# Optimization experiments

Hardware: AMD Instinct MI355X
Metric: run time of the kernel (lower is better)

The kernel has to match this reference:

```python
import jax, jax.numpy as jnp
import numpy as np

N = 200000
E = 6400000
NEG_SLOPE = 0.01  # nn.LeakyReLU default

def _leaky(x):
    return jnp.where(x >= 0, x, NEG_SLOPE * x)

def gcn_conv(x, edge_index, W, b, n):
    # PyG GCNConv: add self-loops, symmetric degree norm, linear, scatter-add, bias
    src, dst = edge_index[0], edge_index[1]
    loops = jnp.arange(n, dtype=src.dtype)
    src = jnp.concatenate([src, loops])
    dst = jnp.concatenate([dst, loops])
    deg = jax.ops.segment_sum(jnp.ones_like(dst, dtype=x.dtype), dst, num_segments=n)
    dinv = jnp.where(deg > 0, jax.lax.rsqrt(deg), 0.0)
    norm = dinv[src] * dinv[dst]                  # [E+N]
    h = x @ W.T                                   # [N,50] linear (no bias yet)
    msg = h[src] * norm[:, None]                  # gather + scale
    out = jax.ops.segment_sum(msg, dst, num_segments=n)  # scatter-add to targets
    return out + b

def setup_inputs() -> dict:
    key = jax.random.key(0)
    ks = jax.random.split(key, 20)
    def w(k, o, i):
        return jax.random.normal(k, (o, i), dtype=jnp.float32) * (1.0 / np.sqrt(i))
    def bvec(k, o):
        return jax.random.normal(k, (o,), dtype=jnp.float32) * 0.01
    inp = {
        'x': jax.random.normal(ks[0], (N, 150), dtype=jnp.float32),
        'edge_index': jax.random.randint(ks[1], (2, E), 0, N, dtype=jnp.int64 if jax.config.jax_enable_x64 else jnp.int32),
        'epsilon': jax.random.normal(ks[2], (N, 10), dtype=jnp.float32),
        'Wg': w(ks[3], 50, 50), 'bg': bvec(ks[4], 50),
        'We1': w(ks[5], 40, 50), 'be1': bvec(ks[6], 40),
        'We2': w(ks[7], 30, 40), 'be2': bvec(ks[8], 30),
        'We3': w(ks[9], 20, 30), 'be3': bvec(ks[10], 20),
        'Wfc': w(ks[11], 10, 10), 'bfc': bvec(ks[12], 10),
        'Wd1': w(ks[13], 20, 10), 'bd1': bvec(ks[14], 20),
        'Wd2': w(ks[15], 40, 20), 'bd2': bvec(ks[16], 40),
        'Wd3': w(ks[17], 50, 40), 'bd3': bvec(ks[18], 50),
    }
    return inp

def reference(x, edge_index, epsilon, Wg, bg, We1, be1, We2, be2, We3, be3,
              Wfc, bfc, Wd1, bd1, Wd2, bd2, Wd3, bd3):
    x1 = x[:, 100:]                                   # [N,50]
    h = gcn_conv(x1, edge_index, Wg, bg, x.shape[0])  # [N,50]
    # encoder
    e = _leaky(h @ We1.T + be1)
    e = _leaky(e @ We2.T + be2)
    e = e @ We3.T + be3                               # [N,20]
    mu, log_var = e[:, :10], e[:, 10:]
    # reparameterization: mu + eps * sqrt(exp(log_var))
    z1 = mu + epsilon * jnp.exp(0.5 * log_var)
    z = jax.nn.relu(z1 @ Wfc.T + bfc)                 # FC
    # decoder
    d = _leaky(z @ Wd1.T + bd1)
    d = _leaky(d @ Wd2.T + bd2)
    mu_prime = jax.nn.sigmoid(d @ Wd3.T + bd3)        # [N,50]
    return (mu_prime, mu, log_var, z)
```

## Files before the change

kernel.cpp:

```cpp
#include <hip/hip_runtime.h>


#define NEG 0.01f
#define GS 64
#define ELLS 64
#define SLICES 16
#define SPILL_CAP 65536

#define DET_ES (1024 * 1024)
#define IS64_THRESH (DET_ES / 2)

typedef int vint4 __attribute__((ext_vector_type(4)));

static __device__ __forceinline__ float bf2f(unsigned short u) {
    return __uint_as_float(((unsigned)u) << 16);
}
static __device__ __forceinline__ float leaky(float a) { return (a >= 0.f) ? a : NEG * a; }

__global__ void k_zero(int* __restrict__ indeg, int* __restrict__ flag, int n) {
    int i = blockIdx.x * 256 + threadIdx.x;
    if (i < n) indeg[i] = 0;
    if (i == 0) { flag[0] = 0; flag[1] = 0; flag[2] = 0; }
}

__global__ void k_detect(const unsigned* __restrict__ x, long xwords,
                         const unsigned* __restrict__ ei, long epairs,
                         int* __restrict__ flag) {
    int gw = (blockIdx.x * 256 + threadIdx.x) >> 6;
    int lane = threadIdx.x & 63;
    int side = gw >> 10;
    int ch = gw & 1023;
    int c = 0;
    if (side == 0) {
        long step = xwords >> 10;
        long base = (long)ch * step;
        if (base + 1024 > xwords) base = xwords > 1024 ? xwords - 1024 : 0;
#pragma unroll
        for (int t = 0; t < 16; t++) {
            long idx = base + t * 64 + lane;
            if (idx < xwords) {
                unsigned w = x[idx];
                if (((w >> 23) & 0xFFu) == 0xFFu || ((w >> 7) & 0xFFu) == 0xFFu) c++;
            }
        }
        for (int k = 32; k; k >>= 1) c += __shfl_xor(c, k);
        if (lane == 0 && c) atomicAdd(&flag[0], c);
    } else {
        long step = epairs >> 10;
        long base = (long)ch * step;
        if (base + 1024 > epairs) base = epairs > 1024 ? epairs - 1024 : 0;
#pragma unroll
        for (int t = 0; t < 16; t++) {
            long idx = base + t * 64 + lane;
            if (idx < epairs && ei[2 * idx + 1] == 0u) c++;
        }
        for (int k = 32; k; k >>= 1) c += __shfl_xor(c, k);
        if (lane == 0 && c) atomicAdd(&flag[1], c);
    }
}

__global__ void k_compact(const unsigned* __restrict__ ei, const int* __restrict__ flag,
                          int* __restrict__ src32, int* __restrict__ dst32, long E) {
    bool is64 = flag[1] > IS64_THRESH;
    long i = (long)blockIdx.x * 256 + threadIdx.x;
    const long stride = 2048L * 256;
    if (is64) {
        const int2* p = (const int2*)ei;
        for (; i < E; i += stride) {
            src32[i] = p[i].x;
            dst32[i] = p[E + i].x;
        }
    } else {
        const int* p = (const int*)ei;
        for (; i < E; i += stride) {
            src32[i] = p[i];
            dst32[i] = p[E + i];
        }
    }
}

__global__ __launch_bounds__(256) void k_build(const int* __restrict__ src32,
                        const int* __restrict__ dst32, int* __restrict__ indeg,
                        int* __restrict__ ebuf, int2* __restrict__ spill,
                        int* __restrict__ flag, int E, int N) {
    int blk = blockIdx.x;
    int pass = blk >> 12;
    int xg = blk & 7;
    int q = (blk & 4095) >> 3;
    int s = pass * 8 + xg;
    int sw = (N + SLICES - 1) / SLICES;
    int nlo = s * sw;
    int nhi = nlo + sw; if (nhi > N) nhi = N;
    const long step = 512L * 256 * 4;
    for (long e0 = ((long)q * 256 + threadIdx.x) * 4; e0 < E; e0 += step) {
        int dv[4];
        if (e0 + 4 <= E) {
            vint4 t = __builtin_nontemporal_load((const vint4*)(dst32 + e0));
            dv[0] = t.x; dv[1] = t.y; dv[2] = t.z; dv[3] = t.w;
        } else {
            for (int k = 0; k < 4; k++) dv[k] = (e0 + k < E) ? dst32[e0 + k] : -1;
        }
#pragma unroll
        for (int k = 0; k < 4; k++) {
            int d = dv[k];
            if (d < nlo || d >= nhi) continue;
            int src = __builtin_nontemporal_load(&src32[e0 + k]);
            if ((unsigned)src >= (unsigned)N) continue;
            int c = atomicAdd(&indeg[d], 1);
            if (c < ELLS) {
                ebuf[(size_t)d * ELLS + c] = src;
            } else {
                int o = atomicAdd(&flag[2], 1);
                if (o < SPILL_CAP) spill[o] = make_int2(src, d);
            }
        }
    }
}

__global__ void k_dinv(const int* __restrict__ indeg, float* __restrict__ dinv, int n) {
    int i = blockIdx.x * 256 + threadIdx.x;
    if (i < n) dinv[i] = rsqrtf(1.0f + (float)indeg[i]);
}

struct CW {
    const void* src[16];
    int off[16];
    int n[16];
};
__global__ void k_convw(CW cw, float* __restrict__ dst, const int* __restrict__ flag) {
    int b = blockIdx.x;
    bool isf = flag[0] > 64;
    const float* sf = (const float*)cw.src[b];
    const unsigned short* sh = (const unsigned short*)cw.src[b];
    float* d = dst + cw.off[b];
    int n = cw.n[b];
    for (int i = threadIdx.x; i < n; i += 256) d[i] = isf ? sf[i] : bf2f(sh[i]);
}

#define O_WG 0
#define O_BG 2500
#define O_WE1 2550
#define O_BE1 4550
#define O_WE2 4590
#define O_BE2 5790
#define O_WE3 5820
#define O_BE3 6420
#define O_WFC 6440
#define O_BFC 6540
#define O_WD1 6550
#define O_BD1 6750
#define O_WD2 6770
#define O_BD2 7570
#define O_WD3 7610
#define O_BD3 9610
#define W_TOT 9660

__global__ __launch_bounds__(256) void k_g(const void* __restrict__ xv,
                                           const float* __restrict__ W,
                                           const float* __restrict__ dinv,
                                           const int* __restrict__ flag,
                                           float* __restrict__ g, int n) {
    int i = blockIdx.x * 256 + threadIdx.x;
    if (i >= n) return;
    bool isf = flag[0] > 64;
    float xr[50];
    if (isf) {
        const float* p = (const float*)xv + (size_t)i * 150 + 100;
#pragma unroll
        for (int k = 0; k < 50; k++) xr[k] = p[k];
    } else {
        const unsigned short* p = (const unsigned short*)xv + (size_t)i * 150 + 100;
#pragma unroll
        for (int k = 0; k < 50; k++) xr[k] = bf2f(p[k]);
    }
    const float* Wg = W + O_WG;
    float di = dinv[i];
    float* gr = g + (size_t)i * GS;
#pragma unroll
    for (int f = 0; f < 50; f += 2) {
        float a0 = 0.f, a1 = 0.f;
#pragma unroll
        for (int p = 0; p < 50; p++) {
            a0 += Wg[f * 50 + p] * xr[p];
            a1 += Wg[(f + 1) * 50 + p] * xr[p];
        }
        gr[f] = a0 * di;
        gr[f + 1] = a1 * di;
    }
}

__global__ __launch_bounds__(256) void k_gather(const float* __restrict__ g,
                                                const int* __restrict__ indeg,
                                                const int* __restrict__ ebuf,
                                                const float* __restrict__ dinv,
                                                const float* __restrict__ W,
                                                float* __restrict__ h1, int n) {
    int wid = threadIdx.x >> 6;
    int lane = threadIdx.x & 63;
    int i = blockIdx.x * 4 + wid;
    if (i >= n) return;
    int fc = lane < 50 ? lane : 49;
    int cnt = indeg[i];
    if (cnt > ELLS) cnt = ELLS;
    float di = dinv[i];
    int ev = (lane < cnt) ? ebuf[(size_t)i * ELLS + lane] : 0;
    float a0 = g[(size_t)i * GS + fc];
    float a1 = 0.f, a2 = 0.f, a3 = 0.f, a4 = 0.f, a5 = 0.f, a6 = 0.f, a7 = 0.f;
    int m = 0;
    for (; m + 7 < cnt; m += 8) {
        int j0 = __shfl(ev, m);
        int j1 = __shfl(ev, m + 1);
        int j2 = __shfl(ev, m + 2);
        int j3 = __shfl(ev, m + 3);
        int j4 = __shfl(ev, m + 4);
        int j5 = __shfl(ev, m + 5);
        int j6 = __shfl(ev, m + 6);
        int j7 = __shfl(ev, m + 7);
        a0 += g[(size_t)j0 * GS + fc];
        a1 += g[(size_t)j1 * GS + fc];
        a2 += g[(size_t)j2 * GS + fc];
        a3 += g[(size_t)j3 * GS + fc];
        a4 += g[(size_t)j4 * GS + fc];
        a5 += g[(size_t)j5 * GS + fc];
        a6 += g[(size_t)j6 * GS + fc];
        a7 += g[(size_t)j7 * GS + fc];
    }
    for (; m < cnt; m++) {
        int j = __shfl(ev, m);
        a0 += g[(size_t)j * GS + fc];
    }
    if (lane < 50) {
        float h = (((a0 + a1) + (a2 + a3)) + ((a4 + a5) + (a6 + a7))) * di + W[O_BG + lane];
        h1[(size_t)i * 50 + lane] = h;
    }
}

__global__ void k_spill(const int2* __restrict__ spill, const int* __restrict__ flag,
                        const float* __restrict__ g, const float* __restrict__ dinv,
                        float* __restrict__ h1) {
    int nov = flag[2];
    if (nov > SPILL_CAP) nov = SPILL_CAP;
    int lane = threadIdx.x & 63;
    int wave = (blockIdx.x * 256 + threadIdx.x) >> 6;
    for (int e = wave; e < nov; e += gridDim.x * 4) {
        int2 sd = spill[e];
        if (lane < 50)
            atomicAdd(&h1[(size_t)sd.y * 50 + lane], g[(size_t)sd.x * GS + lane] * dinv[sd.y]);
    }
}


__global__ __launch_bounds__(256) void k_e1(const float* __restrict__ h1,
                                            const float* __restrict__ W,
                                            float* __restrict__ t1, int n) {
    int i = blockIdx.x * 256 + threadIdx.x;
    if (i >= n) return;
    float v0[50];
    const float2* hr = (const float2*)(h1 + (size_t)i * 50);
#pragma unroll
    for (int p = 0; p < 25; p++) {
        float2 q = hr[p];
        v0[2 * p] = q.x;
        v0[2 * p + 1] = q.y;
    }
    float o[40];
#pragma unroll
    for (int f = 0; f < 40; f++) {
        float a = W[O_BE1 + f];
#pragma unroll
        for (int p = 0; p < 50; p++) a += W[O_WE1 + f * 50 + p] * v0[p];
        o[f] = leaky(a);
    }
    float4* ot = (float4*)(t1 + (size_t)i * 40);
#pragma unroll
    for (int p = 0; p < 10; p++) ot[p] = make_float4(o[4 * p], o[4 * p + 1], o[4 * p + 2], o[4 * p + 3]);
}

__global__ __launch_bounds__(256) void k_e23(const float* __restrict__ t1,
                                             const float* __restrict__ W,
                                             float* __restrict__ out, int n) {
    int i = blockIdx.x * 256 + threadIdx.x;
    if (i >= n) return;
    float v1[40];
    const float4* tr = (const float4*)(t1 + (size_t)i * 40);
#pragma unroll
    for (int p = 0; p < 10; p++) {
        float4 q = tr[p];
        v1[4 * p] = q.x; v1[4 * p + 1] = q.y; v1[4 * p + 2] = q.z; v1[4 * p + 3] = q.w;
    }
    float v2[30];
#pragma unroll
    for (int f = 0; f < 30; f++) {
        float a = W[O_BE2 + f];
#pragma unroll
        for (int p = 0; p < 40; p++) a += W[O_WE2 + f * 40 + p] * v1[p];
        v2[f] = leaky(a);
    }
    float v3[20];
#pragma unroll
    for (int f = 0; f < 20; f++) {
        float a = W[O_BE3 + f];
#pragma unroll
        for (int p = 0; p < 30; p++) a += W[O_WE3 + f * 30 + p] * v2[p];
        v3[f] = a;
    }
    float2* o_mu = (float2*)(out + (size_t)n * 50 + (size_t)i * 10);
    float2* o_lv = (float2*)(out + (size_t)n * 60 + (size_t)i * 10);
#pragma unroll
    for (int p = 0; p < 5; p++) {
        o_mu[p] = make_float2(v3[2 * p], v3[2 * p + 1]);
        o_lv[p] = make_float2(v3[10 + 2 * p], v3[10 + 2 * p + 1]);
    }
}

__global__ __launch_bounds__(256) void k_zfc(float* outb,
                                             const void* __restrict__ epsv,
                                             const float* __restrict__ W,
                                             const int* __restrict__ flag,
                                             float* __restrict__ t3, int n) {
    int i = blockIdx.x * 256 + threadIdx.x;
    if (i >= n) return;
    bool isf = flag[0] > 64;
    float mu[10], lv[10];
    const float2* pm = (const float2*)(outb + (size_t)n * 50 + (size_t)i * 10);
    const float2* pl = (const float2*)(outb + (size_t)n * 60 + (size_t)i * 10);
#pragma unroll
    for (int p = 0; p < 5; p++) {
        float2 a = pm[p]; mu[2 * p] = a.x; mu[2 * p + 1] = a.y;
        float2 b = pl[p]; lv[2 * p] = b.x; lv[2 * p + 1] = b.y;
    }
    float ev[10];
    if (isf) {
        const float* p = (const float*)epsv + (size_t)i * 10;
#pragma unroll
        for (int k = 0; k < 10; k++) ev[k] = p[k];
    } else {
        const unsigned short* p = (const unsigned short*)epsv + (size_t)i * 10;
#pragma unroll
        for (int k = 0; k < 10; k++) ev[k] = bf2f(p[k]);
    }
    float z1[10];
#pragma unroll
    for (int k = 0; k < 10; k++) z1[k] = mu[k] + ev[k] * expf(0.5f * lv[k]);
    float z[10];
#pragma unroll
    for (int f = 0; f < 10; f++) {
        float a = W[O_BFC + f];
#pragma unroll
        for (int p = 0; p < 10; p++) a += W[O_WFC + f * 10 + p] * z1[p];
        z[f] = (a > 0.f) ? a : 0.f;
    }
    float2* o_z = (float2*)(outb + (size_t)n * 70 + (size_t)i * 10);
#pragma unroll
    for (int p = 0; p < 5; p++) o_z[p] = make_float2(z[2 * p], z[2 * p + 1]);
    float d1[20];
#pragma unroll
    for (int f = 0; f < 20; f++) {
        float a = W[O_BD1 + f];
#pragma unroll
        for (int p = 0; p < 10; p++) a += W[O_WD1 + f * 10 + p] * z[p];
        d1[f] = leaky(a);
    }
    float d2[40];
#pragma unroll
    for (int f = 0; f < 40; f++) {
        float a = W[O_BD2 + f];
#pragma unroll
        for (int p = 0; p < 20; p++) a += W[O_WD2 + f * 20 + p] * d1[p];
        d2[f] = leaky(a);
    }
    float4* ot = (float4*)(t3 + (size_t)i * 40);
#pragma unroll
    for (int p = 0; p < 10; p++)
        ot[p] = make_float4(d2[4 * p], d2[4 * p + 1], d2[4 * p + 2], d2[4 * p + 3]);
}

__global__ __launch_bounds__(256) void k_d3(const float* __restrict__ t3,
                                            const float* __restrict__ W,
                                            float* __restrict__ out, int n) {
    int i = blockIdx.x * 256 + threadIdx.x;
    if (i >= n) return;
    float d2[40];
    const float4* tr = (const float4*)(t3 + (size_t)i * 40);
#pragma unroll
    for (int p = 0; p < 10; p++) {
        float4 q = tr[p];
        d2[4 * p] = q.x; d2[4 * p + 1] = q.y; d2[4 * p + 2] = q.z; d2[4 * p + 3] = q.w;
    }
    float o[50];
#pragma unroll
    for (int f = 0; f < 50; f++) {
        float a = W[O_BD3 + f];
#pragma unroll
        for (int p = 0; p < 40; p++) a += W[O_WD3 + f * 40 + p] * d2[p];
        o[f] = 1.f / (1.f + expf(-a));
    }
    float2* om = (float2*)(out + (size_t)i * 50);
#pragma unroll
    for (int p = 0; p < 25; p++) om[p] = make_float2(o[2 * p], o[2 * p + 1]);
}

extern "C" void kernel_launch(void* const* d_in, const int* in_sizes, int n_in,
                              void* d_out, int out_size, void* d_ws, size_t ws_size,
                              hipStream_t stream) {
    const int N = in_sizes[0] / 150;
    const int E = in_sizes[1] / 2;

    char* w = (char*)d_ws;
    auto alloc = [&](size_t bytes) {
        void* p = (void*)w;
        w += (bytes + 255) & ~(size_t)255;
        return p;
    };
    int* indeg = (int*)alloc((size_t)N * 4);
    int* flag = (int*)alloc(256);
    float* dinv = (float*)alloc((size_t)N * 4);
    float* Wall = (float*)alloc((size_t)W_TOT * 4);
    int2* spill = (int2*)alloc((size_t)SPILL_CAP * 8);
    float* g = (float*)alloc((size_t)N * GS * 4);
    float* h1 = (float*)alloc((size_t)N * 50 * 4);
    int* ebuf = (int*)alloc((size_t)N * ELLS * 4);

    int* dst32;
    int* src32;
    if (2L * E <= (long)N * GS) {
        dst32 = (int*)g;
        src32 = (int*)g + E;
    } else {
        dst32 = (int*)alloc((size_t)E * 4);
        src32 = (int*)alloc((size_t)E * 4);
    }

    float* t1 = g;
    float* t3 = h1;

    CW cw;
    static const int wn[16] = {2500, 50, 2000, 40, 1200, 30, 600, 20,
                               100, 10, 200, 20, 800, 40, 2000, 50};
    static const int wo[16] = {O_WG, O_BG, O_WE1, O_BE1, O_WE2, O_BE2, O_WE3, O_BE3,
                               O_WFC, O_BFC, O_WD1, O_BD1, O_WD2, O_BD2, O_WD3, O_BD3};
    for (int k = 0; k < 16; k++) {
        cw.src[k] = d_in[3 + k];
        cw.off[k] = wo[k];
        cw.n[k] = wn[k];
    }

    int nbN = (N + 255) / 256;

    k_zero<<<nbN, 256, 0, stream>>>(indeg, flag, N);
    k_detect<<<512, 256, 0, stream>>>((const unsigned*)d_in[0], (long)N * 75,
                                      (const unsigned*)d_in[1], (long)E, flag);
    k_compact<<<2048, 256, 0, stream>>>((const unsigned*)d_in[1], flag, src32, dst32, (long)E);
    k_build<<<8192, 256, 0, stream>>>(src32, dst32, indeg, ebuf, spill, flag, E, N);
    k_dinv<<<nbN, 256, 0, stream>>>(indeg, dinv, N);
    k_convw<<<16, 256, 0, stream>>>(cw, Wall, flag);
    k_g<<<nbN, 256, 0, stream>>>(d_in[0], Wall, dinv, flag, g, N);
    k_gather<<<(N + 3) / 4, 256, 0, stream>>>(g, indeg, ebuf, dinv, Wall, h1, N);
    k_spill<<<64, 256, 0, stream>>>(spill, flag, g, dinv, h1);
    k_e1<<<nbN, 256, 0, stream>>>(h1, Wall, t1, N);
    k_e23<<<nbN, 256, 0, stream>>>(t1, Wall, (float*)d_out, N);
    k_zfc<<<nbN, 256, 0, stream>>>((float*)d_out, d_in[2], Wall, flag, t3, N);
    k_d3<<<nbN, 256, 0, stream>>>(t3, Wall, (float*)d_out, N);
}
```

Measured before the change: 1.028 ms.

## Partition edges into destination buckets before building the ELL adjacency

Replaces the compact step and the sliced build, which rescanned the whole destination array once per slice, with three steps. A histogram kernel counts edges per destination bucket, a tiny scan computes bucket offsets, and a partition kernel stages edges in LDS and writes (src,dst) pairs into contiguous per-bucket regions. The build then runs in two launches, each walking only the edges of its own buckets, so the repeated global reads of the edge list go away. The cost is an extra pass over the destination indices, more launches and block-level synchronisation in the partition kernel, which uses about 64KB of LDS per block.

```diff
diff --git a/kernel.cpp b/kernel.cpp
--- a/kernel.cpp
+++ b/kernel.cpp
@@ -4,23 +4,29 @@
 #define NEG 0.01f
 #define GS 64
 #define ELLS 64
-#define SLICES 16
+#define NB 16
 #define SPILL_CAP 65536
 
 #define DET_ES (1024 * 1024)
 #define IS64_THRESH (DET_ES / 2)
 
-typedef int vint4 __attribute__((ext_vector_type(4)));
+#define META_INTS 1024
+
+typedef int vint2 __attribute__((ext_vector_type(2)));
 
 static __device__ __forceinline__ float bf2f(unsigned short u) {
     return __uint_as_float(((unsigned)u) << 16);
 }
 static __device__ __forceinline__ float leaky(float a) { return (a >= 0.f) ? a : NEG * a; }
 
-__global__ void k_zero(int* __restrict__ indeg, int* __restrict__ flag, int n) {
+__global__ void k_zero(int* __restrict__ indeg, int* __restrict__ flag,
+                       int* __restrict__ meta, int n) {
     int i = blockIdx.x * 256 + threadIdx.x;
     if (i < n) indeg[i] = 0;
-    if (i == 0) { flag[0] = 0; flag[1] = 0; flag[2] = 0; }
+    if (blockIdx.x == 0) {
+        for (int j = threadIdx.x; j < META_INTS; j += 256) meta[j] = 0;
+        if (threadIdx.x == 0) { flag[0] = 0; flag[1] = 0; flag[2] = 0; }
+    }
 }
 
 __global__ void k_detect(const unsigned* __restrict__ x, long xwords,
@@ -59,60 +65,128 @@
     }
 }
 
-__global__ void k_compact(const unsigned* __restrict__ ei, const int* __restrict__ flag,
-                          int* __restrict__ src32, int* __restrict__ dst32, long E) {
+__global__ __launch_bounds__(256) void k_hist(const int* __restrict__ ei,
+                                              const int* __restrict__ flag,
+                                              int* __restrict__ meta, int E, int N) {
+    __shared__ int lh[NB];
+    if (threadIdx.x < NB) lh[threadIdx.x] = 0;
+    __syncthreads();
     bool is64 = flag[1] > IS64_THRESH;
-    long i = (long)blockIdx.x * 256 + threadIdx.x;
-    const long stride = 2048L * 256;
+    unsigned usw = ((unsigned)N + NB - 1) / NB;
+    const long stride = 1024L * 256;
     if (is64) {
         const int2* p = (const int2*)ei;
-        for (; i < E; i += stride) {
-            src32[i] = p[i].x;
-            dst32[i] = p[E + i].x;
+        for (long e = (long)blockIdx.x * 256 + threadIdx.x; e < E; e += stride) {
+            int d = p[E + e].x;
+            if ((unsigned)d < (unsigned)N) atomicAdd(&lh[(unsigned)d / usw], 1);
         }
     } else {
-        const int* p = (const int*)ei;
-        for (; i < E; i += stride) {
-            src32[i] = p[i];
-            dst32[i] = p[E + i];
-        }
-    }
-}
-
-__global__ __launch_bounds__(256) void k_build(const int* __restrict__ src32,
-                        const int* __restrict__ dst32, int* __restrict__ indeg,
-                        int* __restrict__ ebuf, int2* __restrict__ spill,
-                        int* __restrict__ flag, int E, int N) {
-    int blk = blockIdx.x;
-    int pass = blk >> 12;
-    int xg = blk & 7;
-    int q = (blk & 4095) >> 3;
-    int s = pass * 8 + xg;
-    int sw = (N + SLICES - 1) / SLICES;
-    int nlo = s * sw;
-    int nhi = nlo + sw; if (nhi > N) nhi = N;
-    const long step = 512L * 256 * 4;
-    for (long e0 = ((long)q * 256 + threadIdx.x) * 4; e0 < E; e0 += step) {
-        int dv[4];
-        if (e0 + 4 <= E) {
-            vint4 t = __builtin_nontemporal_load((const vint4*)(dst32 + e0));
-            dv[0] = t.x; dv[1] = t.y; dv[2] = t.z; dv[3] = t.w;
+        for (long e = (long)blockIdx.x * 256 + threadIdx.x; e < E; e += stride) {
+            int d = ei[E + e];
+            if ((unsigned)d < (unsigned)N) atomicAdd(&lh[(unsigned)d / usw], 1);
+        }
+    }
+    __syncthreads();
+    if (threadIdx.x < NB && lh[threadIdx.x]) atomicAdd(&meta[threadIdx.x * 16], lh[threadIdx.x]);
+}
+
+__global__ void k_scan(int* __restrict__ meta) {
+    if (threadIdx.x == 0) {
+        int acc = 0;
+        for (int k = 0; k < NB; k++) {
+            int c = meta[k * 16];
+            meta[256 + k] = acc;
+            meta[512 + k * 16] = acc;
+            acc += c;
+            meta[288 + k] = acc;
+        }
+    }
+}
+
+__global__ __launch_bounds__(256) void k_part(const int* __restrict__ ei,
+                                              const int* __restrict__ flag,
+                                              int* __restrict__ meta,
+                                              int2* __restrict__ bucket, int E, int N) {
+    __shared__ int2 buf[NB][512];
+    __shared__ int lcnt[NB];
+    __shared__ int lbase;
+    if (threadIdx.x < NB) lcnt[threadIdx.x] = 0;
+    __syncthreads();
+    bool is64 = flag[1] > IS64_THRESH;
+    unsigned usw = ((unsigned)N + NB - 1) / NB;
+    int nsteps = (E + 2048 * 256 - 1) / (2048 * 256);
+    for (int step = 0; step < nsteps; step++) {
+        long e = (long)(step * 2048 + blockIdx.x) * 256 + threadIdx.x;
+        int b = -1;
+        int2 sd;
+        if (e < E) {
+            int src, d;
+            if (is64) {
+                const int2* p = (const int2*)ei;
+                src = p[e].x;
+                d = p[E + e].x;
+            } else {
+                src = ei[e];
+                d = ei[E + e];
+            }
+            if ((unsigned)d < (unsigned)N) {
+                b = (int)((unsigned)d / usw);
+                sd = make_int2(src, d);
+            }
+        }
+        if (b >= 0) {
+            int p = atomicAdd(&lcnt[b], 1);
+            buf[b][p] = sd;
+        }
+        __syncthreads();
+        for (int k = 0; k < NB; k++) {
+            int cnt = lcnt[k];
+            if (cnt >= 256) {
+                if (threadIdx.x == 0) lbase = atomicAdd(&meta[512 + k * 16], 256);
+                __syncthreads();
+                bucket[lbase + threadIdx.x] = buf[k][threadIdx.x];
+                int rem = cnt - 256;
+                int2 r;
+                if (threadIdx.x < rem) r = buf[k][256 + threadIdx.x];
+                __syncthreads();
+                if (threadIdx.x < rem) buf[k][threadIdx.x] = r;
+                if (threadIdx.x == 0) lcnt[k] = rem;
+                __syncthreads();
+            }
+        }
+    }
+    for (int k = 0; k < NB; k++) {
+        int cnt = lcnt[k];
+        if (cnt > 0) {
+            if (threadIdx.x == 0) lbase = atomicAdd(&meta[512 + k * 16], cnt);
+            __syncthreads();
+            if (threadIdx.x < cnt) bucket[lbase + threadIdx.x] = buf[k][threadIdx.x];
+            __syncthreads();
+        }
+    }
+}
+
+__global__ __launch_bounds__(256) void k_build2(const int2* __restrict__ bucket,
+                                                const int* __restrict__ meta,
+                                                int* __restrict__ indeg,
+                                                int* __restrict__ ebuf,
+                                                int2* __restrict__ spill,
+                                                int* __restrict__ flag, int N, int pass) {
+    int s = pass * 8 + (blockIdx.x & 7);
+    int q = blockIdx.x >> 3;
+    int lo = meta[256 + s];
+    int hi = meta[288 + s];
+    for (int idx = lo + q * 256 + threadIdx.x; idx < hi; idx += 512 * 256) {
+        vint2 t = __builtin_nontemporal_load((const vint2*)&bucket[idx]);
+        int src = t.x;
+        int d = t.y;
+        if ((unsigned)src >= (unsigned)N) continue;
+        int c = atomicAdd(&indeg[d], 1);
+        if (c < ELLS) {
+            ebuf[(size_t)d * ELLS + c] = src;
         } else {
-            for (int k = 0; k < 4; k++) dv[k] = (e0 + k < E) ? dst32[e0 + k] : -1;
-        }
-#pragma unroll
-        for (int k = 0; k < 4; k++) {
-            int d = dv[k];
-            if (d < nlo || d >= nhi) continue;
-            int src = __builtin_nontemporal_load(&src32[e0 + k]);
-            if ((unsigned)src >= (unsigned)N) continue;
-            int c = atomicAdd(&indeg[d], 1);
-            if (c < ELLS) {
-                ebuf[(size_t)d * ELLS + c] = src;
-            } else {
-                int o = atomicAdd(&flag[2], 1);
-                if (o < SPILL_CAP) spill[o] = make_int2(src, d);
-            }
+            int o = atomicAdd(&flag[2], 1);
+            if (o < SPILL_CAP) spill[o] = make_int2(src, d);
         }
     }
 }
@@ -414,6 +488,7 @@
     };
     int* indeg = (int*)alloc((size_t)N * 4);
     int* flag = (int*)alloc(256);
+    int* meta = (int*)alloc((size_t)META_INTS * 4);
     float* dinv = (float*)alloc((size_t)N * 4);
     float* Wall = (float*)alloc((size_t)W_TOT * 4);
     int2* spill = (int2*)alloc((size_t)SPILL_CAP * 8);
@@ -421,14 +496,11 @@
     float* h1 = (float*)alloc((size_t)N * 50 * 4);
     int* ebuf = (int*)alloc((size_t)N * ELLS * 4);
 
-    int* dst32;
-    int* src32;
-    if (2L * E <= (long)N * GS) {
-        dst32 = (int*)g;
-        src32 = (int*)g + E;
+    int2* bucket;
+    if ((size_t)E * 8 <= (size_t)N * GS * 4 + (size_t)N * 50 * 4) {
+        bucket = (int2*)g;
     } else {
-        dst32 = (int*)alloc((size_t)E * 4);
-        src32 = (int*)alloc((size_t)E * 4);
+        bucket = (int2*)alloc((size_t)E * 8);
     }
 
     float* t1 = g;
@@ -447,11 +519,14 @@
 
     int nbN = (N + 255) / 256;
 
-    k_zero<<<nbN, 256, 0, stream>>>(indeg, flag, N);
+    k_zero<<<nbN, 256, 0, stream>>>(indeg, flag, meta, N);
     k_detect<<<512, 256, 0, stream>>>((const unsigned*)d_in[0], (long)N * 75,
                                       (const unsigned*)d_in[1], (long)E, flag);
-    k_compact<<<2048, 256, 0, stream>>>((const unsigned*)d_in[1], flag, src32, dst32, (long)E);
-    k_build<<<8192, 256, 0, stream>>>(src32, dst32, indeg, ebuf, spill, flag, E, N);
+    k_hist<<<1024, 256, 0, stream>>>((const int*)d_in[1], flag, meta, E, N);
+    k_scan<<<1, 64, 0, stream>>>(meta);
+    k_part<<<2048, 256, 0, stream>>>((const int*)d_in[1], flag, meta, bucket, E, N);
+    k_build2<<<4096, 256, 0, stream>>>(bucket, meta, indeg, ebuf, spill, flag, N, 0);
+    k_build2<<<4096, 256, 0, stream>>>(bucket, meta, indeg, ebuf, spill, flag, N, 1);
     k_dinv<<<nbN, 256, 0, stream>>>(indeg, dinv, N);
     k_convw<<<16, 256, 0, stream>>>(cw, Wall, flag);
     k_g<<<nbN, 256, 0, stream>>>(d_in[0], Wall, dinv, flag, g, N);
```

Result: slower. 1.086 ms (+5.7%).
